# Performance work log

Hardware: AMD Instinct MI355X
Metric: run time of the kernel (lower is better)

Reference implementation:

```python
import jax, jax.numpy as jnp
import numpy as np

T, B, C = 1024, 8, 256
H, F = 8, 512
D = C // H  # head dim = 32
EPS = 1e-5


def _layernorm(x, g, b):
    mu = jnp.mean(x, axis=-1, keepdims=True)
    var = jnp.var(x, axis=-1, keepdims=True)
    return (x - mu) * jax.lax.rsqrt(var + EPS) * g + b


def setup_inputs() -> dict:
    key = jax.random.key(0)
    ks = jax.random.split(key, 12)
    s = 0.02
    return {
        "x_TBC": jax.random.normal(ks[0], (T, B, C), jnp.float32),
        "key_padding_mask": jnp.zeros((B, T), dtype=bool),
        "edge_bias": jax.random.normal(ks[1], (B, H, T, T), jnp.float32),
        "ln1_g": jnp.ones((C,), jnp.float32),
        "ln1_b": jnp.zeros((C,), jnp.float32),
        "ln2_g": jnp.ones((C,), jnp.float32),
        "ln2_b": jnp.zeros((C,), jnp.float32),
        "w_qkv": jax.random.normal(ks[2], (3 * C, C), jnp.float32) * s,
        "b_qkv": jnp.zeros((3 * C,), jnp.float32),
        "w_o": jax.random.normal(ks[3], (C, C), jnp.float32) * s,
        "b_o": jnp.zeros((C,), jnp.float32),
        "w1": jax.random.normal(ks[4], (F, C), jnp.float32) * s,
        "b1": jnp.zeros((F,), jnp.float32),
        "w2": jax.random.normal(ks[5], (C, F), jnp.float32) * s,
        "b2": jnp.zeros((C,), jnp.float32),
    }


def _attn(y, key_padding_mask, edge_bias, w_qkv, b_qkv, w_o, b_o):
    # y: [T,B,C]
    qkv = jnp.einsum('tbc,ec->tbe', y, w_qkv) + b_qkv  # [T,B,3C]
    q, k, v = jnp.split(qkv, 3, axis=-1)
    def heads(z):  # [T,B,C] -> [B,H,T,D]
        return z.reshape(T, B, H, D).transpose(1, 2, 0, 3)
    q, k, v = heads(q), heads(k), heads(v)
    scale = 1.0 / jnp.sqrt(jnp.asarray(D, jnp.float32))
    scores = jnp.einsum('bhqd,bhkd->bhqk', q * scale, k) + edge_bias
    neg = jnp.asarray(-1e9, scores.dtype)
    scores = jnp.where(key_padding_mask[:, None, None, :], neg, scores)
    probs = jax.nn.softmax(scores, axis=-1)
    o = jnp.einsum('bhqk,bhkd->bhqd', probs, v)  # [B,H,T,D]
    o = o.transpose(2, 0, 1, 3).reshape(T, B, C)
    return jnp.einsum('tbc,ec->tbe', o, w_o) + b_o


def reference(x_TBC, key_padding_mask, edge_bias, ln1_g, ln1_b, ln2_g, ln2_b,
              w_qkv, b_qkv, w_o, b_o, w1, b1, w2, b2):
    # pre-LN: LN -> attn(edge bias) -> residual, LN -> FFN -> residual
    y = _layernorm(x_TBC, ln1_g, ln1_b)
    y = _attn(y, key_padding_mask, edge_bias, w_qkv, b_qkv, w_o, b_o)
    x = x_TBC + y
    y = _layernorm(x, ln2_g, ln2_b)
    y = jax.nn.gelu(jnp.einsum('tbc,fc->tbf', y, w1) + b1, approximate=False)
    y = jnp.einsum('tbf,cf->tbc', y, w2) + b2
    return x + y
```

## Files before the change

kernel.cpp:

```cpp
#include <hip/hip_runtime.h>
#include <hip/hip_bf16.h>
#include <cmath>

#define T_DIM 1024
#define B_DIM 8
#define C_DIM 256
#define H_DIM 8
#define D_DIM 32
#define F_DIM 512

typedef __attribute__((ext_vector_type(4))) float f32x4;
typedef __attribute__((ext_vector_type(8))) short bf16x8;

static __device__ __forceinline__ unsigned short f2bf(float f) {
    union { float f; unsigned u; } v; v.f = f;
    unsigned r = v.u + 0x7fff + ((v.u >> 16) & 1);
    return (unsigned short)(r >> 16);
}

static __device__ __forceinline__ void gload_lds16(const void* g, void* l) {
    __builtin_amdgcn_global_load_lds(
        (const __attribute__((address_space(1))) unsigned int*)g,
        (__attribute__((address_space(3))) unsigned int*)l,
        16, 0, 0);
}

__global__ __launch_bounds__(256) void convert_weights(const float* __restrict__ wqkv,
                                                       const float* __restrict__ wo,
                                                       const float* __restrict__ w1,
                                                       const float* __restrict__ w2,
                                                       unsigned short* __restrict__ dst)
{
    int e = blockIdx.x * 256 + threadIdx.x;
    const float* src; int off;
    if (e < 196608)      { src = wqkv; off = 0; }
    else if (e < 262144) { src = wo;   off = 196608; }
    else if (e < 393216) { src = w1;   off = 262144; }
    else                 { src = w2;   off = 393216; }
    dst[e] = f2bf(src[e - off]);
}

__global__ __launch_bounds__(256) void ln_bf16(const float* __restrict__ x,
                                               const float* __restrict__ g,
                                               const float* __restrict__ bta,
                                               unsigned short* __restrict__ y)
{
    int row  = blockIdx.x * 4 + (threadIdx.x >> 6);
    int lane = threadIdx.x & 63;
    float4 v = ((const float4*)(x + (size_t)row * C_DIM))[lane];
    float s  = v.x + v.y + v.z + v.w;
    float ss = v.x * v.x + v.y * v.y + v.z * v.z + v.w * v.w;
#pragma unroll
    for (int off = 1; off < 64; off <<= 1) {
        s  += __shfl_xor(s, off);
        ss += __shfl_xor(ss, off);
    }
    float mu   = s * (1.0f / C_DIM);
    float var  = ss * (1.0f / C_DIM) - mu * mu;
    float rstd = rsqrtf(var + 1e-5f);
    float4 gv = ((const float4*)g)[lane];
    float4 bv = ((const float4*)bta)[lane];
    ushort4 o;
    o.x = f2bf((v.x - mu) * rstd * gv.x + bv.x);
    o.y = f2bf((v.y - mu) * rstd * gv.y + bv.y);
    o.z = f2bf((v.z - mu) * rstd * gv.z + bv.z);
    o.w = f2bf((v.w - mu) * rstd * gv.w + bv.w);
    ((ushort4*)(y + (size_t)row * C_DIM))[lane] = o;
}

template<int EPI>
__global__ __launch_bounds__(256) void gemm_mfma(const unsigned short* __restrict__ A,
                                                 const unsigned short* __restrict__ W,
                                                 const float* __restrict__ bias,
                                                 const float* __restrict__ R,
                                                 void* __restrict__ outv,
                                                 int N, int K)
{
    __shared__ __align__(16) unsigned short A_s[128 * 64];
    __shared__ __align__(16) unsigned short W_s[64 * 64];
    int tid  = threadIdx.x;
    int lane = tid & 63;
    int wv   = tid >> 6;
    int l15  = lane & 15, lg = lane >> 4;
    int row0 = blockIdx.y * 128;
    int col0 = blockIdx.x * 64;

    f32x4 acc[2][4] = {};
    for (int k0 = 0; k0 < K; k0 += 64) {
#pragma unroll
        for (int i = 0; i < 4; i++) {
            int u = (wv * 4 + i) * 64 + lane;
            int r = u >> 3, c = u & 7;
            gload_lds16(A + (size_t)(row0 + r) * K + k0 + ((c ^ (r & 7)) * 8),
                        &A_s[(size_t)(wv * 4 + i) * 512]);
        }
#pragma unroll
        for (int j = 0; j < 2; j++) {
            int u = (wv * 2 + j) * 64 + lane;
            int r = u >> 3, c = u & 7;
            gload_lds16(W + (size_t)(col0 + r) * K + k0 + ((c ^ (r & 7)) * 8),
                        &W_s[(size_t)(wv * 2 + j) * 512]);
        }
        __syncthreads();
#pragma unroll
        for (int kk = 0; kk < 2; kk++) {
            bf16x8 af[2], wf[4];
#pragma unroll
            for (int mb = 0; mb < 2; mb++) {
                int rowa = wv * 32 + mb * 16 + l15;
                af[mb] = *(const bf16x8*)&A_s[rowa * 64 + (((kk * 4 + lg) ^ (l15 & 7)) * 8)];
            }
#pragma unroll
            for (int nb = 0; nb < 4; nb++) {
                int roww = nb * 16 + l15;
                wf[nb] = *(const bf16x8*)&W_s[roww * 64 + (((kk * 4 + lg) ^ (l15 & 7)) * 8)];
            }
#pragma unroll
            for (int mb = 0; mb < 2; mb++)
#pragma unroll
                for (int nb = 0; nb < 4; nb++)
                    acc[mb][nb] = __builtin_amdgcn_mfma_f32_16x16x32_bf16(af[mb], wf[nb], acc[mb][nb], 0, 0, 0);
        }
        __syncthreads();
    }
#pragma unroll
    for (int nb = 0; nb < 4; nb++) {
        int c = col0 + nb * 16 + l15;
        float bv = bias[c];
#pragma unroll
        for (int mb = 0; mb < 2; mb++) {
#pragma unroll
            for (int r = 0; r < 4; r++) {
                int rowm = row0 + wv * 32 + mb * 16 + lg * 4 + r;
                float v = acc[mb][nb][r] + bv;
                if (EPI == 1) v = 0.5f * v * (1.0f + erff(v * 0.70710678118654752f));
                if (EPI == 2) {
                    v += R[(size_t)rowm * N + c];
                    ((float*)outv)[(size_t)rowm * N + c] = v;
                } else {
                    ((unsigned short*)outv)[(size_t)rowm * N + c] = f2bf(v);
                }
            }
        }
    }
}

__global__ __launch_bounds__(256) void attn_mfma(const unsigned short* __restrict__ qkv,
                                                 const float* __restrict__ bias,
                                                 const unsigned char* __restrict__ mask,
                                                 unsigned short* __restrict__ o)
{
    __shared__ __align__(16) unsigned short K_s[64 * 32];
    __shared__ unsigned short Vt_s[32][72];
    __shared__ unsigned short P_s[4][16][72];
    __shared__ unsigned char m_s[64];

    int tid  = threadIdx.x;
    int lane = tid & 63;
    int wv   = tid >> 6;
    int l15  = lane & 15, lg = lane >> 4;
    int bh = blockIdx.y, b = bh >> 3, hh = bh & 7;
    int q0 = blockIdx.x * 64;
    int qw = q0 + wv * 16;
    const float scale = 0.17677669529663687f;

    bf16x8 qf = *(const bf16x8*)(qkv + ((size_t)(qw + l15) * B_DIM + b) * 768 + hh * 32 + lg * 8);

    int krow = wv * 16 + (lane >> 2);
    int kc   = lane & 3;
    int kswz = (kc ^ (krow & 3)) * 8;
    const unsigned short* kfp = &K_s[l15 * 32 + ((lg ^ (l15 & 3)) * 8)];

    const float* bptr = bias + ((size_t)bh * T_DIM + q0 + wv * 16 + l15) * T_DIM + lg * 4;

    float m_run = -INFINITY, l_run = 0.0f;
    f32x4 oacc[2] = {};

    for (int k0 = 0; k0 < T_DIM; k0 += 64) {
        f32x4 bb0 = *(const f32x4*)(bptr + k0);
        f32x4 bb1 = *(const f32x4*)(bptr + k0 + 16);
        f32x4 bb2 = *(const f32x4*)(bptr + k0 + 32);
        f32x4 bb3 = *(const f32x4*)(bptr + k0 + 48);
        gload_lds16(qkv + ((size_t)(k0 + krow) * B_DIM + b) * 768 + 256 + hh * 32 + kswz,
                    &K_s[(size_t)wv * 512]);
#pragma unroll
        for (int i = 0; i < 4; i++) {
            int p = tid + i * 256;
            int kv = p >> 4, dp = (p & 15) * 2;
            uint32_t vv = *(const uint32_t*)(qkv + ((size_t)(k0 + kv) * B_DIM + b) * 768 + 512 + hh * 32 + dp);
            Vt_s[dp][kv]     = (unsigned short)(vv & 0xffff);
            Vt_s[dp + 1][kv] = (unsigned short)(vv >> 16);
        }
        if (tid < 64) m_s[tid] = mask[b * T_DIM + k0 + tid];
        __syncthreads();

        float sv[4][4];
        float tmax = -INFINITY;
        const f32x4 bb[4] = {bb0, bb1, bb2, bb3};
#pragma unroll
        for (int kb = 0; kb < 4; kb++) {
            bf16x8 kf = *(const bf16x8*)(kfp + kb * 512);
            f32x4 z = {0.0f, 0.0f, 0.0f, 0.0f};
            f32x4 sc = __builtin_amdgcn_mfma_f32_16x16x32_bf16(kf, qf, z, 0, 0, 0);
            uint32_t mw = *(const uint32_t*)&m_s[kb * 16 + lg * 4];
#pragma unroll
            for (int r = 0; r < 4; r++) {
                float s = sc[r] * scale + bb[kb][r];
                if ((mw >> (8 * r)) & 0xff) s = -1e9f;
                sv[kb][r] = s;
                tmax = fmaxf(tmax, s);
            }
        }
        tmax = fmaxf(tmax, __shfl_xor(tmax, 16));
        tmax = fmaxf(tmax, __shfl_xor(tmax, 32));
        float m_new = fmaxf(m_run, tmax);
        float corr = __expf(m_run - m_new);
        m_run = m_new;

        float ls = 0.0f;
#pragma unroll
        for (int kb = 0; kb < 4; kb++) {
            float p0 = __expf(sv[kb][0] - m_new);
            float p1 = __expf(sv[kb][1] - m_new);
            float p2 = __expf(sv[kb][2] - m_new);
            float p3 = __expf(sv[kb][3] - m_new);
            ls += (p0 + p1) + (p2 + p3);
            uint2 pw;
            pw.x = (uint32_t)f2bf(p0) | ((uint32_t)f2bf(p1) << 16);
            pw.y = (uint32_t)f2bf(p2) | ((uint32_t)f2bf(p3) << 16);
            *(uint2*)&P_s[wv][l15][kb * 16 + lg * 4] = pw;
        }
        ls += __shfl_xor(ls, 16);
        ls += __shfl_xor(ls, 32);
        l_run = l_run * corr + ls;
#pragma unroll
        for (int db = 0; db < 2; db++)
#pragma unroll
            for (int r = 0; r < 4; r++) oacc[db][r] *= corr;

#pragma unroll
        for (int h = 0; h < 2; h++) {
            bf16x8 pf = *(const bf16x8*)&P_s[wv][l15][h * 32 + lg * 8];
#pragma unroll
            for (int db = 0; db < 2; db++) {
                bf16x8 vf = *(const bf16x8*)&Vt_s[db * 16 + l15][h * 32 + lg * 8];
                oacc[db] = __builtin_amdgcn_mfma_f32_16x16x32_bf16(vf, pf, oacc[db], 0, 0, 0);
            }
        }
        __syncthreads();
    }

    float inv = 1.0f / l_run;
#pragma unroll
    for (int db = 0; db < 2; db++) {
        ushort4 ov;
        ov.x = f2bf(oacc[db][0] * inv);
        ov.y = f2bf(oacc[db][1] * inv);
        ov.z = f2bf(oacc[db][2] * inv);
        ov.w = f2bf(oacc[db][3] * inv);
        *(ushort4*)(o + ((size_t)(qw + l15) * B_DIM + b) * C_DIM + hh * 32 + db * 16 + lg * 4) = ov;
    }
}

extern "C" void kernel_launch(void* const* d_in, const int* in_sizes, int n_in,
                              void* d_out, int out_size, void* d_ws, size_t ws_size,
                              hipStream_t stream)
{
    const float* x            = (const float*)d_in[0];
    const unsigned char* mask = (const unsigned char*)d_in[1];
    const float* bias         = (const float*)d_in[2];
    const float* ln1g         = (const float*)d_in[3];
    const float* ln1b         = (const float*)d_in[4];
    const float* ln2g         = (const float*)d_in[5];
    const float* ln2b         = (const float*)d_in[6];
    const float* wqkv         = (const float*)d_in[7];
    const float* bqkv         = (const float*)d_in[8];
    const float* wo           = (const float*)d_in[9];
    const float* bo           = (const float*)d_in[10];
    const float* w1           = (const float*)d_in[11];
    const float* b1           = (const float*)d_in[12];
    const float* w2           = (const float*)d_in[13];
    const float* b2           = (const float*)d_in[14];
    float* out = (float*)d_out;
    char* ws   = (char*)d_ws;

    unsigned short* wbf     = (unsigned short*)ws;
    unsigned short* wqkv_bf = wbf;
    unsigned short* wo_bf   = wbf + 196608;
    unsigned short* w1_bf   = wbf + 262144;
    unsigned short* w2_bf   = wbf + 393216;
    unsigned short* y_bf    = (unsigned short*)(ws + (1u << 20));
    unsigned short* qkv_bf  = (unsigned short*)(ws + 5u * (1u << 20));
    unsigned short* o_bf    = (unsigned short*)(ws + 17u * (1u << 20));
    float*          x1      = (float*)(ws + 21u * (1u << 20));
    unsigned short* h_bf    = (unsigned short*)(ws + 29u * (1u << 20));

    const int M = T_DIM * B_DIM;

    convert_weights<<<2048, 256, 0, stream>>>(wqkv, wo, w1, w2, wbf);
    ln_bf16<<<M / 4, 256, 0, stream>>>(x, ln1g, ln1b, y_bf);
    gemm_mfma<0><<<dim3(768 / 64, M / 128), 256, 0, stream>>>(y_bf, wqkv_bf, bqkv, nullptr, qkv_bf, 768, 256);
    attn_mfma<<<dim3(T_DIM / 64, B_DIM * H_DIM), 256, 0, stream>>>(qkv_bf, bias, mask, o_bf);
    gemm_mfma<2><<<dim3(256 / 64, M / 128), 256, 0, stream>>>(o_bf, wo_bf, bo, x, x1, 256, 256);
    ln_bf16<<<M / 4, 256, 0, stream>>>(x1, ln2g, ln2b, y_bf);
    gemm_mfma<1><<<dim3(512 / 64, M / 128), 256, 0, stream>>>(y_bf, w1_bf, b1, nullptr, h_bf, 512, 256);
    gemm_mfma<2><<<dim3(256 / 64, M / 128), 256, 0, stream>>>(h_bf, w2_bf, b2, x1, out, 256, 512);
}
```

Before: 138.6 us.

## Restructure attention to independent per-wave heads and store residual as bf16

The attention kernel now gives each wave its own (batch, head) pair over 16 queries, in 128-thread blocks. Each wave loads K fragments and the mask directly from global memory into registers and transposes V into a private LDS buffer, so the block-wide barriers go away. It also adds s_setprio around the MFMA sections. Separately, the intermediate residual x1 is stored as bf16 instead of fp32, with a new LayerNorm variant and GEMM epilogue that read it. This cuts memory traffic but lowers the precision of the residual that feeds the output.

Measured after the change: 175.4 us. 1.27x slower.

```diff
diff --git a/kernel.cpp b/kernel.cpp
--- a/kernel.cpp
+++ b/kernel.cpp
@@ -16,6 +16,10 @@
     union { float f; unsigned u; } v; v.f = f;
     unsigned r = v.u + 0x7fff + ((v.u >> 16) & 1);
     return (unsigned short)(r >> 16);
+}
+static __device__ __forceinline__ float bf2f(unsigned short h) {
+    union { unsigned u; float f; } v; v.u = ((unsigned)h) << 16;
+    return v.f;
 }
 
 static __device__ __forceinline__ void gload_lds16(const void* g, void* l) {
@@ -68,11 +72,40 @@
     ((ushort4*)(y + (size_t)row * C_DIM))[lane] = o;
 }
 
+__global__ __launch_bounds__(256) void ln_bf16i(const unsigned short* __restrict__ x,
+                                                const float* __restrict__ g,
+                                                const float* __restrict__ bta,
+                                                unsigned short* __restrict__ y)
+{
+    int row  = blockIdx.x * 4 + (threadIdx.x >> 6);
+    int lane = threadIdx.x & 63;
+    ushort4 hv = ((const ushort4*)(x + (size_t)row * C_DIM))[lane];
+    float4 v = {bf2f(hv.x), bf2f(hv.y), bf2f(hv.z), bf2f(hv.w)};
+    float s  = v.x + v.y + v.z + v.w;
+    float ss = v.x * v.x + v.y * v.y + v.z * v.z + v.w * v.w;
+#pragma unroll
+    for (int off = 1; off < 64; off <<= 1) {
+        s  += __shfl_xor(s, off);
+        ss += __shfl_xor(ss, off);
+    }
+    float mu   = s * (1.0f / C_DIM);
+    float var  = ss * (1.0f / C_DIM) - mu * mu;
+    float rstd = rsqrtf(var + 1e-5f);
+    float4 gv = ((const float4*)g)[lane];
+    float4 bv = ((const float4*)bta)[lane];
+    ushort4 o;
+    o.x = f2bf((v.x - mu) * rstd * gv.x + bv.x);
+    o.y = f2bf((v.y - mu) * rstd * gv.y + bv.y);
+    o.z = f2bf((v.z - mu) * rstd * gv.z + bv.z);
+    o.w = f2bf((v.w - mu) * rstd * gv.w + bv.w);
+    ((ushort4*)(y + (size_t)row * C_DIM))[lane] = o;
+}
+
 template<int EPI>
 __global__ __launch_bounds__(256) void gemm_mfma(const unsigned short* __restrict__ A,
                                                  const unsigned short* __restrict__ W,
                                                  const float* __restrict__ bias,
-                                                 const float* __restrict__ R,
+                                                 const void* __restrict__ Rv,
                                                  void* __restrict__ outv,
                                                  int N, int K)
 {
@@ -134,8 +167,9 @@
                 int rowm = row0 + wv * 32 + mb * 16 + lg * 4 + r;
                 float v = acc[mb][nb][r] + bv;
                 if (EPI == 1) v = 0.5f * v * (1.0f + erff(v * 0.70710678118654752f));
-                if (EPI == 2) {
-                    v += R[(size_t)rowm * N + c];
+                if (EPI == 2) v += ((const float*)Rv)[(size_t)rowm * N + c];
+                if (EPI == 3) {
+                    v += bf2f(((const unsigned short*)Rv)[(size_t)rowm * N + c]);
                     ((float*)outv)[(size_t)rowm * N + c] = v;
                 } else {
                     ((unsigned short*)outv)[(size_t)rowm * N + c] = f2bf(v);
@@ -145,72 +179,67 @@
     }
 }
 
-__global__ __launch_bounds__(256) void attn_mfma(const unsigned short* __restrict__ qkv,
+__global__ __launch_bounds__(128) void attn_mfma(const unsigned short* __restrict__ qkv,
                                                  const float* __restrict__ bias,
                                                  const unsigned char* __restrict__ mask,
                                                  unsigned short* __restrict__ o)
 {
-    __shared__ __align__(16) unsigned short K_s[64 * 32];
-    __shared__ unsigned short Vt_s[32][72];
-    __shared__ unsigned short P_s[4][16][72];
-    __shared__ unsigned char m_s[64];
+    __shared__ unsigned short Vt_s[2][32][40];
+    __shared__ unsigned short P_s[2][16][72];
 
     int tid  = threadIdx.x;
     int lane = tid & 63;
-    int wv   = tid >> 6;
+    int w    = tid >> 6;
     int l15  = lane & 15, lg = lane >> 4;
-    int bh = blockIdx.y, b = bh >> 3, hh = bh & 7;
-    int q0 = blockIdx.x * 64;
-    int qw = q0 + wv * 16;
+    int bh = blockIdx.y * 2 + w, b = bh >> 3, hh = bh & 7;
+    int q0 = blockIdx.x * 16;
     const float scale = 0.17677669529663687f;
 
-    bf16x8 qf = *(const bf16x8*)(qkv + ((size_t)(qw + l15) * B_DIM + b) * 768 + hh * 32 + lg * 8);
-
-    int krow = wv * 16 + (lane >> 2);
-    int kc   = lane & 3;
-    int kswz = (kc ^ (krow & 3)) * 8;
-    const unsigned short* kfp = &K_s[l15 * 32 + ((lg ^ (l15 & 3)) * 8)];
-
-    const float* bptr = bias + ((size_t)bh * T_DIM + q0 + wv * 16 + l15) * T_DIM + lg * 4;
+    bf16x8 qf = *(const bf16x8*)(qkv + ((size_t)(q0 + l15) * B_DIM + b) * 768 + hh * 32 + lg * 8);
+    const float* bptr = bias + ((size_t)bh * T_DIM + q0 + l15) * T_DIM + lg * 4;
 
     float m_run = -INFINITY, l_run = 0.0f;
     f32x4 oacc[2] = {};
 
     for (int k0 = 0; k0 < T_DIM; k0 += 64) {
-        f32x4 bb0 = *(const f32x4*)(bptr + k0);
-        f32x4 bb1 = *(const f32x4*)(bptr + k0 + 16);
-        f32x4 bb2 = *(const f32x4*)(bptr + k0 + 32);
-        f32x4 bb3 = *(const f32x4*)(bptr + k0 + 48);
-        gload_lds16(qkv + ((size_t)(k0 + krow) * B_DIM + b) * 768 + 256 + hh * 32 + kswz,
-                    &K_s[(size_t)wv * 512]);
-#pragma unroll
-        for (int i = 0; i < 4; i++) {
-            int p = tid + i * 256;
-            int kv = p >> 4, dp = (p & 15) * 2;
-            uint32_t vv = *(const uint32_t*)(qkv + ((size_t)(k0 + kv) * B_DIM + b) * 768 + 512 + hh * 32 + dp);
-            Vt_s[dp][kv]     = (unsigned short)(vv & 0xffff);
-            Vt_s[dp + 1][kv] = (unsigned short)(vv >> 16);
-        }
-        if (tid < 64) m_s[tid] = mask[b * T_DIM + k0 + tid];
-        __syncthreads();
+        f32x4 bb[4];
+        bf16x8 kf[4];
+        uint32_t mw[4];
+#pragma unroll
+        for (int kb = 0; kb < 4; kb++) {
+            bb[kb] = *(const f32x4*)(bptr + k0 + kb * 16);
+            kf[kb] = *(const bf16x8*)(qkv + ((size_t)(k0 + kb * 16 + l15) * B_DIM + b) * 768
+                                      + 256 + hh * 32 + lg * 8);
+            mw[kb] = *(const uint32_t*)(mask + (size_t)b * T_DIM + k0 + kb * 16 + lg * 4);
+        }
+#pragma unroll
+        for (int j = 0; j < 8; j++) {
+            int p = j * 64 + lane;
+            int kv2 = p >> 4, dp = (p & 15) * 2;
+            const unsigned short* vp = qkv + ((size_t)(k0 + kv2 * 2) * B_DIM + b) * 768
+                                       + 512 + hh * 32 + dp;
+            uint32_t v0 = *(const uint32_t*)vp;
+            uint32_t v1 = *(const uint32_t*)(vp + 768 * B_DIM);
+            *(uint32_t*)&Vt_s[w][dp][kv2 * 2]     = (v0 & 0xffffu) | (v1 << 16);
+            *(uint32_t*)&Vt_s[w][dp + 1][kv2 * 2] = (v0 >> 16) | (v1 & 0xffff0000u);
+        }
 
         float sv[4][4];
         float tmax = -INFINITY;
-        const f32x4 bb[4] = {bb0, bb1, bb2, bb3};
+        __builtin_amdgcn_s_setprio(1);
 #pragma unroll
         for (int kb = 0; kb < 4; kb++) {
-            bf16x8 kf = *(const bf16x8*)(kfp + kb * 512);
             f32x4 z = {0.0f, 0.0f, 0.0f, 0.0f};
-            f32x4 sc = __builtin_amdgcn_mfma_f32_16x16x32_bf16(kf, qf, z, 0, 0, 0);
-            uint32_t mw = *(const uint32_t*)&m_s[kb * 16 + lg * 4];
+            f32x4 sc = __builtin_amdgcn_mfma_f32_16x16x32_bf16(kf[kb], qf, z, 0, 0, 0);
 #pragma unroll
             for (int r = 0; r < 4; r++) {
                 float s = sc[r] * scale + bb[kb][r];
-                if ((mw >> (8 * r)) & 0xff) s = -1e9f;
+                if ((mw[kb] >> (8 * r)) & 0xff) s = -1e9f;
                 sv[kb][r] = s;
                 tmax = fmaxf(tmax, s);
             }
         }
+        __builtin_amdgcn_s_setprio(0);
         tmax = fmaxf(tmax, __shfl_xor(tmax, 16));
         tmax = fmaxf(tmax, __shfl_xor(tmax, 32));
         float m_new = fmaxf(m_run, tmax);
@@ -228,7 +257,7 @@
             uint2 pw;
             pw.x = (uint32_t)f2bf(p0) | ((uint32_t)f2bf(p1) << 16);
             pw.y = (uint32_t)f2bf(p2) | ((uint32_t)f2bf(p3) << 16);
-            *(uint2*)&P_s[wv][l15][kb * 16 + lg * 4] = pw;
+            *(uint2*)&P_s[w][l15][kb * 16 + lg * 4] = pw;
         }
         ls += __shfl_xor(ls, 16);
         ls += __shfl_xor(ls, 32);
@@ -238,16 +267,17 @@
 #pragma unroll
             for (int r = 0; r < 4; r++) oacc[db][r] *= corr;
 
+        __builtin_amdgcn_s_setprio(1);
 #pragma unroll
         for (int h = 0; h < 2; h++) {
-            bf16x8 pf = *(const bf16x8*)&P_s[wv][l15][h * 32 + lg * 8];
+            bf16x8 pf = *(const bf16x8*)&P_s[w][l15][h * 32 + lg * 8];
 #pragma unroll
             for (int db = 0; db < 2; db++) {
-                bf16x8 vf = *(const bf16x8*)&Vt_s[db * 16 + l15][h * 32 + lg * 8];
+                bf16x8 vf = *(const bf16x8*)&Vt_s[w][db * 16 + l15][h * 32 + lg * 8];
                 oacc[db] = __builtin_amdgcn_mfma_f32_16x16x32_bf16(vf, pf, oacc[db], 0, 0, 0);
             }
         }
-        __syncthreads();
+        __builtin_amdgcn_s_setprio(0);
     }
 
     float inv = 1.0f / l_run;
@@ -258,7 +288,7 @@
         ov.y = f2bf(oacc[db][1] * inv);
         ov.z = f2bf(oacc[db][2] * inv);
         ov.w = f2bf(oacc[db][3] * inv);
-        *(ushort4*)(o + ((size_t)(qw + l15) * B_DIM + b) * C_DIM + hh * 32 + db * 16 + lg * 4) = ov;
+        *(ushort4*)(o + ((size_t)(q0 + l15) * B_DIM + b) * C_DIM + hh * 32 + db * 16 + lg * 4) = ov;
     }
 }
 
@@ -292,7 +322,7 @@
     unsigned short* y_bf    = (unsigned short*)(ws + (1u << 20));
     unsigned short* qkv_bf  = (unsigned short*)(ws + 5u * (1u << 20));
     unsigned short* o_bf    = (unsigned short*)(ws + 17u * (1u << 20));
-    float*          x1      = (float*)(ws + 21u * (1u << 20));
+    unsigned short* x1_bf   = (unsigned short*)(ws + 21u * (1u << 20));
     unsigned short* h_bf    = (unsigned short*)(ws + 29u * (1u << 20));
 
     const int M = T_DIM * B_DIM;
@@ -300,9 +330,9 @@
     convert_weights<<<2048, 256, 0, stream>>>(wqkv, wo, w1, w2, wbf);
     ln_bf16<<<M / 4, 256, 0, stream>>>(x, ln1g, ln1b, y_bf);
     gemm_mfma<0><<<dim3(768 / 64, M / 128), 256, 0, stream>>>(y_bf, wqkv_bf, bqkv, nullptr, qkv_bf, 768, 256);
-    attn_mfma<<<dim3(T_DIM / 64, B_DIM * H_DIM), 256, 0, stream>>>(qkv_bf, bias, mask, o_bf);
-    gemm_mfma<2><<<dim3(256 / 64, M / 128), 256, 0, stream>>>(o_bf, wo_bf, bo, x, x1, 256, 256);
-    ln_bf16<<<M / 4, 256, 0, stream>>>(x1, ln2g, ln2b, y_bf);
+    attn_mfma<<<dim3(T_DIM / 16, B_DIM * H_DIM / 2), 128, 0, stream>>>(qkv_bf, bias, mask, o_bf);
+    gemm_mfma<2><<<dim3(256 / 64, M / 128), 256, 0, stream>>>(o_bf, wo_bf, bo, x, x1_bf, 256, 256);
+    ln_bf16i<<<M / 4, 256, 0, stream>>>(x1_bf, ln2g, ln2b, y_bf);
     gemm_mfma<1><<<dim3(512 / 64, M / 128), 256, 0, stream>>>(y_bf, w1_bf, b1, nullptr, h_bf, 512, 256);
-    gemm_mfma<2><<<dim3(256 / 64, M / 128), 256, 0, stream>>>(h_bf, w2_bf, b2, x1, out, 256, 512);
-}
+    gemm_mfma<3><<<dim3(256 / 64, M / 128), 256, 0, stream>>>(h_bf, w2_bf, b2, x1_bf, out, 256, 512);
+}
```
